# Kernel tuning notes

Measured on AMD Instinct MI355X. Metric: run time of the kernel, lower is better.

The kernel has to match this reference:

```python
import jax, jax.numpy as jnp
import numpy as np

SEQ_LENGTH = 4096
HIDDEN = 4096
N_HEADS = 32
N_KV = 2
HEAD_DIM = 128
ROT_DIM = 64  # head_dim // 2, rotary applied to first half
FFN = 13696
EPS = 1e-5


def rope_cache(seq_len):
    theta = 1.0 / (10000.0 ** (jnp.arange(0, ROT_DIM, 2, dtype=jnp.float32) / ROT_DIM))  # [32]
    idx = jnp.arange(seq_len, dtype=jnp.float32)
    freqs = jnp.outer(idx, theta)  # [seq, 32]
    return jnp.stack([jnp.cos(freqs), jnp.sin(freqs)], axis=-1)  # [seq, 32, 2]


def apply_rope(x, rope):
    # x: [sq, b, nh, 128]; rope: [sq, b, 32, 2]
    sq, b, nh, hn = x.shape
    xr = x[..., :ROT_DIM].reshape(sq, b, nh, ROT_DIM // 2, 2)
    x0, x1 = xr[..., 0], xr[..., 1]
    cos = rope[:, :, None, :, 0]
    sin = rope[:, :, None, :, 1]
    out = jnp.stack([x0 * cos - x1 * sin, x1 * cos + x0 * sin], axis=-1)
    out = out.reshape(sq, b, nh, ROT_DIM)
    return jnp.concatenate([out, x[..., ROT_DIM:]], axis=-1)


def rmsnorm(x, w):
    var = jnp.mean(jnp.square(x), axis=-1, keepdims=True)
    return x * jax.lax.rsqrt(var + EPS) * w


def setup_inputs() -> dict:
    key = jax.random.key(0)
    ks = jax.random.split(key, 12)
    B, L = 32, SEQ_LENGTH - 1
    s = 0.02
    return {
        'hidden_states': jax.random.normal(ks[0], (1, B, HIDDEN), jnp.float32),
        'position_ids': jax.random.randint(ks[1], (B, 1), 0, SEQ_LENGTH),
        'attention_mask': jnp.zeros((B, 1, 1, SEQ_LENGTH), dtype=bool),
        'past_k': jax.random.normal(ks[2], (L, B, N_KV, HEAD_DIM), jnp.float32),
        'past_v': jax.random.normal(ks[3], (L, B, N_KV, HEAD_DIM), jnp.float32),
        'w_ln1': 1.0 + s * jax.random.normal(ks[4], (HIDDEN,), jnp.float32),
        'w_qkv': s * jax.random.normal(ks[5], (HIDDEN + 2 * N_KV * HEAD_DIM, HIDDEN), jnp.float32),
        'b_qkv': s * jax.random.normal(ks[6], (HIDDEN + 2 * N_KV * HEAD_DIM,), jnp.float32),
        'w_dense': s * jax.random.normal(ks[7], (HIDDEN, HIDDEN), jnp.float32),
        'w_ln2': 1.0 + s * jax.random.normal(ks[8], (HIDDEN,), jnp.float32),
        'w_fc1': s * jax.random.normal(ks[9], (2 * FFN, HIDDEN), jnp.float32),
        'w_fc2': s * jax.random.normal(ks[10], (HIDDEN, FFN), jnp.float32),
    }


def reference(hidden_states, position_ids, attention_mask, past_k, past_v,
              w_ln1, w_qkv, b_qkv, w_dense, w_ln2, w_fc1, w_fc2):
    sq, B, _ = hidden_states.shape
    # rotary_pos_emb(SEQ_LENGTH)[position_ids].transpose(0, 1)
    rope = rope_cache(SEQ_LENGTH)[position_ids]          # [B, sq, 32, 2]
    rope = jnp.transpose(rope, (1, 0, 2, 3))             # [sq, B, 32, 2]

    # --- self attention ---
    residual = hidden_states
    x = rmsnorm(hidden_states, w_ln1)
    qkv = jnp.einsum('sbh,oh->sbo', x, w_qkv) + b_qkv    # [sq, B, 4608]
    q = qkv[..., :HIDDEN].reshape(sq, B, N_HEADS, HEAD_DIM)
    k = qkv[..., HIDDEN:HIDDEN + N_KV * HEAD_DIM].reshape(sq, B, N_KV, HEAD_DIM)
    v = qkv[..., HIDDEN + N_KV * HEAD_DIM:].reshape(sq, B, N_KV, HEAD_DIM)
    q = apply_rope(q, rope)
    k = apply_rope(k, rope)

    k_cache = jnp.concatenate([past_k, k], axis=0)       # [L+sq, B, 2, 128]
    v_cache = jnp.concatenate([past_v, v], axis=0)

    rep = N_HEADS // N_KV
    kx = jnp.repeat(k_cache, rep, axis=2)                # [sk, B, 32, 128]
    vx = jnp.repeat(v_cache, rep, axis=2)

    scale = 1.0 / jnp.sqrt(jnp.float32(HEAD_DIM))
    scores = jnp.einsum('qbhd,kbhd->bhqk', q, kx) * scale  # [B, 32, sq, sk]
    scores = jnp.where(attention_mask, jnp.float32(-1e9), scores)
    probs = jax.nn.softmax(scores, axis=-1)
    ctx = jnp.einsum('bhqk,kbhd->qbhd', probs, vx).reshape(sq, B, HIDDEN)
    attn_out = jnp.einsum('sbh,oh->sbo', ctx, w_dense)

    hidden = residual + attn_out

    # --- MLP (SwiGLU) ---
    residual = hidden
    x = rmsnorm(hidden, w_ln2)
    h = jnp.einsum('sbh,oh->sbo', x, w_fc1)              # [sq, B, 2*FFN]
    a, b = jnp.split(h, 2, axis=-1)
    h = jax.nn.silu(a) * b
    mlp_out = jnp.einsum('sbf,of->sbo', h, w_fc2)
    hidden = residual + mlp_out

    return hidden, k_cache[1:], v_cache[1:]
```

## Files before the change

kernel.cpp:

```cpp
#include <hip/hip_runtime.h>


constexpr int B    = 32;
constexpr int HID  = 4096;
constexpr int NKV  = 2;
constexpr int HD   = 128;
constexpr int QKVN = 4608;
constexpr int FFN  = 13696;
constexpr int FC1N = 2 * FFN;
constexpr int PAST = 4095;
constexpr int NSPL = 8;

constexpr size_t OFF_X1    = 0;
constexpr size_t OFF_QKVP  = OFF_X1    + (size_t)B * HID;
constexpr size_t OFF_Q     = OFF_QKVP  + 4ull * B * QKVN;
constexpr size_t OFF_KN    = OFF_Q     + (size_t)B * HID;
constexpr size_t OFF_VN    = OFF_KN    + (size_t)B * NKV * HD;
constexpr size_t OFF_CTXP  = OFF_VN    + (size_t)B * NKV * HD;
constexpr size_t OFF_ML    = OFF_CTXP  + (size_t)B * NKV * NSPL * 16 * HD;
constexpr size_t OFF_CTX   = OFF_ML    + (size_t)B * NKV * NSPL * 16 * 2;
constexpr size_t OFF_DENSP = OFF_CTX   + (size_t)B * HID;
constexpr size_t OFF_HID   = OFF_DENSP + 4ull * B * HID;
constexpr size_t OFF_X2    = OFF_HID   + (size_t)B * HID;
constexpr size_t OFF_H1    = OFF_X2    + (size_t)B * HID;
constexpr size_t OFF_HG    = OFF_H1    + 2ull * B * FC1N;
constexpr size_t OFF_FC2P  = OFF_HG    + (size_t)B * FFN;

__global__ __launch_bounds__(256) void k_rmsnorm(
    const float* __restrict__ x, const float* __restrict__ w,
    float* __restrict__ out)
{
  const int b = blockIdx.x, t = threadIdx.x;
  const float* xr = x + (size_t)b * HID;
  float4 v[4];
  float ss = 0.f;
#pragma unroll
  for (int r = 0; r < 4; r++) {
    v[r] = *(const float4*)&xr[(t + r * 256) * 4];
    ss += v[r].x * v[r].x + v[r].y * v[r].y + v[r].z * v[r].z + v[r].w * v[r].w;
  }
#pragma unroll
  for (int off = 32; off; off >>= 1) ss += __shfl_xor(ss, off);
  __shared__ float wsum[4];
  if ((t & 63) == 0) wsum[t >> 6] = ss;
  __syncthreads();
  const float tot = wsum[0] + wsum[1] + wsum[2] + wsum[3];
  const float inv = rsqrtf(tot * (1.f / HID) + 1e-5f);
  float* orow = out + (size_t)b * HID;
#pragma unroll
  for (int r = 0; r < 4; r++) {
    const int i = (t + r * 256) * 4;
    const float4 wv = *(const float4*)&w[i];
    float4 o;
    o.x = v[r].x * inv * wv.x;
    o.y = v[r].y * inv * wv.y;
    o.z = v[r].z * inv * wv.z;
    o.w = v[r].w * inv * wv.w;
    *(float4*)&orow[i] = o;
  }
}

__global__ __launch_bounds__(256) void k_resid_norm(
    const float* __restrict__ hs, const float* __restrict__ dpart,
    const float* __restrict__ w, float* __restrict__ hid,
    float* __restrict__ out)
{
  const int b = blockIdx.x, t = threadIdx.x;
  float4 v[4];
  float ss = 0.f;
#pragma unroll
  for (int r = 0; r < 4; r++) {
    const int i = (t + r * 256) * 4;
    float4 a = *(const float4*)&hs[(size_t)b * HID + i];
#pragma unroll
    for (int s = 0; s < 4; s++) {
      const float4 p = *(const float4*)&dpart[((size_t)s * B + b) * HID + i];
      a.x += p.x; a.y += p.y; a.z += p.z; a.w += p.w;
    }
    v[r] = a;
    *(float4*)&hid[(size_t)b * HID + i] = a;
    ss += a.x * a.x + a.y * a.y + a.z * a.z + a.w * a.w;
  }
#pragma unroll
  for (int off = 32; off; off >>= 1) ss += __shfl_xor(ss, off);
  __shared__ float wsum[4];
  if ((t & 63) == 0) wsum[t >> 6] = ss;
  __syncthreads();
  const float tot = wsum[0] + wsum[1] + wsum[2] + wsum[3];
  const float inv = rsqrtf(tot * (1.f / HID) + 1e-5f);
#pragma unroll
  for (int r = 0; r < 4; r++) {
    const int i = (t + r * 256) * 4;
    const float4 wv = *(const float4*)&w[i];
    float4 o;
    o.x = v[r].x * inv * wv.x;
    o.y = v[r].y * inv * wv.y;
    o.z = v[r].z * inv * wv.z;
    o.w = v[r].w * inv * wv.w;
    *(float4*)&out[(size_t)b * HID + i] = o;
  }
}

__global__ __launch_bounds__(256, 2) void k_gemv32(
    const float* __restrict__ A, const float* __restrict__ W,
    const float* __restrict__ bias, float* __restrict__ outp,
    int N, int K, int ksplit_len)
{
  __shared__ __align__(16) float xs[8192];
  const int t = threadIdx.x;
  const int wv = t >> 6, l = t & 63;
  const int olane = l >> 2, kq = l & 3;
  const int bh = wv & 1, kh = wv >> 1;
  const int o_base = blockIdx.x * 64;
  const int kb = blockIdx.y * ksplit_len;
  const int ke = kb + ksplit_len;

  float acc[4][16];
#pragma unroll
  for (int j = 0; j < 4; j++)
#pragma unroll
    for (int bb = 0; bb < 16; bb++) acc[j][bb] = 0.f;

  const float* Wr[4];
#pragma unroll
  for (int j = 0; j < 4; j++)
    Wr[j] = W + (size_t)(o_base + olane + 16 * j) * K;

  for (int kc = kb; kc < ke; kc += 256) {
    const int csz = min(256, ke - kc);
    const int c4n = csz >> 2;
    __syncthreads();
#pragma unroll
    for (int r = 0; r < 8; r++) {
      const int f = t + r * 256;
      const int b = f >> 6, c4 = f & 63;
      if (c4 < c4n)
        *(float4*)&xs[b * 256 + c4 * 4] =
            *(const float4*)&A[(size_t)b * K + kc + c4 * 4];
    }
    __syncthreads();
#pragma unroll
    for (int i = 0; i < 8; i++) {
      const int kl = kh * 128 + i * 16 + kq * 4;
      if (kl < csz) {
        float4 w4[4];
#pragma unroll
        for (int j = 0; j < 4; j++) w4[j] = *(const float4*)&Wr[j][kc + kl];
#pragma unroll
        for (int bb = 0; bb < 16; bb++) {
          const float4 xv = *(const float4*)&xs[(bh * 16 + bb) * 256 + kl];
#pragma unroll
          for (int j = 0; j < 4; j++)
            acc[j][bb] += w4[j].x * xv.x + w4[j].y * xv.y +
                          w4[j].z * xv.z + w4[j].w * xv.w;
        }
      }
    }
  }
#pragma unroll
  for (int j = 0; j < 4; j++)
#pragma unroll
    for (int bb = 0; bb < 16; bb++) {
      float v = acc[j][bb];
      v += __shfl_xor(v, 1);
      v += __shfl_xor(v, 2);
      acc[j][bb] = v;
    }
  __syncthreads();
  if (kq == 0) {
#pragma unroll
    for (int j = 0; j < 4; j++)
#pragma unroll
      for (int bb = 0; bb < 16; bb++)
        xs[(wv * 64 + olane + 16 * j) * 16 + bb] = acc[j][bb];
  }
  __syncthreads();
#pragma unroll
  for (int r = 0; r < 8; r++) {
    const int pair = t + r * 256;
    const int rl = pair >> 5, b = pair & 31;
    const int bh2 = b >> 4, bb2 = b & 15;
    float v = xs[(bh2 * 64 + rl) * 16 + bb2] +
              xs[((bh2 + 2) * 64 + rl) * 16 + bb2];
    if (bias != nullptr && blockIdx.y == 0) v += bias[o_base + rl];
    outp[((size_t)blockIdx.y * B + b) * N + o_base + rl] = v;
  }
}

__global__ __launch_bounds__(256) void k_qkv_rope(
    const float* __restrict__ qkvp, const int* __restrict__ pos_ids,
    float* __restrict__ qo, float* __restrict__ ko, float* __restrict__ vo)
{
  const int idx = blockIdx.x * 256 + threadIdx.x;
  const int b = idx / 1152;
  const int f4 = idx - b * 1152;
  const int o = f4 * 4;
  float4 v = {0.f, 0.f, 0.f, 0.f};
#pragma unroll
  for (int s = 0; s < 4; s++) {
    const float4 p = *(const float4*)&qkvp[((size_t)s * B + b) * QKVN + o];
    v.x += p.x; v.y += p.y; v.z += p.z; v.w += p.w;
  }
  const int d = o & 127;
  if (o < HID + NKV * HD && d < 64) {
    const int pos = pos_ids[b];
    const int i0 = d >> 1;
    const float f0 = pos * __expf(-0.28782313662425572f * i0);
    const float f1 = pos * __expf(-0.28782313662425572f * (i0 + 1));
    float c0, s0, c1, s1;
    sincosf(f0, &s0, &c0);
    sincosf(f1, &s1, &c1);
    float4 r;
    r.x = v.x * c0 - v.y * s0;
    r.y = v.y * c0 + v.x * s0;
    r.z = v.z * c1 - v.w * s1;
    r.w = v.w * c1 + v.z * s1;
    v = r;
  }
  if (o < HID) {
    *(float4*)&qo[(size_t)b * HID + o] = v;
  } else if (o < HID + NKV * HD) {
    *(float4*)&ko[(size_t)b * (NKV * HD) + (o - HID)] = v;
  } else {
    *(float4*)&vo[(size_t)b * (NKV * HD) + (o - HID - NKV * HD)] = v;
  }
}

__global__ __launch_bounds__(256) void k_cache_copy(
    const float4* __restrict__ pk, const float4* __restrict__ pv,
    const float4* __restrict__ kn, const float4* __restrict__ vn,
    float4* __restrict__ ok, float4* __restrict__ ov)
{
  constexpr int ROW4 = B * NKV * HD / 4;
  constexpr long long MAIN = (long long)(PAST - 1) * ROW4;
  constexpr long long TAIL = ROW4;
  const long long total = 2 * (MAIN + TAIL);
  for (long long i = (long long)blockIdx.x * 256 + threadIdx.x; i < total;
       i += (long long)gridDim.x * 256) {
    if (i < MAIN) {
      ok[i] = pk[i + ROW4];
    } else if (i < MAIN + TAIL) {
      ok[i] = kn[i - MAIN];
    } else if (i < 2 * MAIN + TAIL) {
      const long long j = i - (MAIN + TAIL);
      ov[j] = pv[j + ROW4];
    } else {
      const long long j = i - (MAIN + TAIL);
      ov[j] = vn[i - (2 * MAIN + TAIL)];
    }
  }
}

__global__ __launch_bounds__(256) void k_attn_partial(
    const float* __restrict__ q, const float* __restrict__ past_k,
    const float* __restrict__ past_v, const float* __restrict__ kn,
    const float* __restrict__ vn, float* __restrict__ ctxp,
    float* __restrict__ mlbuf)
{
  __shared__ __align__(16) float qs[16 * 128];
  __shared__ __align__(16) float sc[512 * 20];
  const int t = threadIdx.x;
  const int split = blockIdx.x, kvh = blockIdx.y, b = blockIdx.z;

#pragma unroll
  for (int r = 0; r < 2; r++) {
    const int f4 = t + r * 256;
    const int hh = f4 >> 5, d4 = f4 & 31;
    *(float4*)&qs[hh * 128 + d4 * 4] =
        *(const float4*)&q[(size_t)b * HID + (kvh * 16 + hh) * HD + d4 * 4];
  }
  __syncthreads();

  const float scale = 0.08838834764831845f;
#pragma unroll
  for (int pi = 0; pi < 2; pi++) {
    const int pl = t + pi * 256;
    const int pg = split * 512 + pl;
    const float* kr = (pg < PAST)
        ? &past_k[(size_t)((pg * B + b) * NKV + kvh) * HD]
        : &kn[(size_t)(b * NKV + kvh) * HD];
    float s[16];
#pragma unroll
    for (int hh = 0; hh < 16; hh++) s[hh] = 0.f;
#pragma unroll 4
    for (int d4 = 0; d4 < 32; d4++) {
      const float4 kv = *(const float4*)&kr[d4 * 4];
#pragma unroll
      for (int hh = 0; hh < 16; hh++) {
        const float4 q4 = *(const float4*)&qs[hh * 128 + d4 * 4];
        s[hh] += q4.x * kv.x + q4.y * kv.y + q4.z * kv.z + q4.w * kv.w;
      }
    }
#pragma unroll
    for (int hh = 0; hh < 16; hh++) sc[pl * 20 + hh] = s[hh] * scale;
  }
  __syncthreads();

  {
    const int hh = t >> 4, l16 = t & 15;
    float m = -1e30f;
    for (int jj = 0; jj < 32; jj++)
      m = fmaxf(m, sc[(l16 + jj * 16) * 20 + hh]);
#pragma unroll
    for (int off = 8; off; off >>= 1) m = fmaxf(m, __shfl_xor(m, off));
    float lsum = 0.f;
    for (int jj = 0; jj < 32; jj++) {
      const int p = l16 + jj * 16;
      const float e = __expf(sc[p * 20 + hh] - m);
      sc[p * 20 + hh] = e;
      lsum += e;
    }
#pragma unroll
    for (int off = 8; off; off >>= 1) lsum += __shfl_xor(lsum, off);
    if (l16 == 0) {
      const size_t base =
          (((size_t)(b * NKV + kvh) * NSPL + split) * 16 + hh) * 2;
      mlbuf[base] = m;
      mlbuf[base + 1] = lsum;
    }
  }
  __syncthreads();

  const int hg = t >> 7, d = t & 127;
  float acc[8];
#pragma unroll
  for (int k8 = 0; k8 < 8; k8++) acc[k8] = 0.f;
  for (int pl = 0; pl < 512; pl++) {
    const int pg = split * 512 + pl;
    const float vd = (pg < PAST)
        ? past_v[(size_t)((pg * B + b) * NKV + kvh) * HD + d]
        : vn[(size_t)(b * NKV + kvh) * HD + d];
    const float4 e0 = *(const float4*)&sc[pl * 20 + hg * 8];
    const float4 e1 = *(const float4*)&sc[pl * 20 + hg * 8 + 4];
    acc[0] += e0.x * vd; acc[1] += e0.y * vd;
    acc[2] += e0.z * vd; acc[3] += e0.w * vd;
    acc[4] += e1.x * vd; acc[5] += e1.y * vd;
    acc[6] += e1.z * vd; acc[7] += e1.w * vd;
  }
#pragma unroll
  for (int k8 = 0; k8 < 8; k8++) {
    const size_t idx =
        (((size_t)(b * NKV + kvh) * NSPL + split) * 16 + hg * 8 + k8) * HD + d;
    ctxp[idx] = acc[k8];
  }
}

__global__ __launch_bounds__(128) void k_attn_merge(
    const float* __restrict__ ctxp, const float* __restrict__ mlbuf,
    float* __restrict__ ctx)
{
  const int h = blockIdx.x, b = blockIdx.y, d = threadIdx.x;
  const int kvh = h >> 4, hh = h & 15;
  float ms[NSPL], ls[NSPL];
  float M = -1e30f;
#pragma unroll
  for (int s = 0; s < NSPL; s++) {
    const size_t base = (((size_t)(b * NKV + kvh) * NSPL + s) * 16 + hh) * 2;
    ms[s] = mlbuf[base];
    ls[s] = mlbuf[base + 1];
    M = fmaxf(M, ms[s]);
  }
  float L = 0.f, val = 0.f;
#pragma unroll
  for (int s = 0; s < NSPL; s++) {
    const float w = __expf(ms[s] - M);
    L += ls[s] * w;
    val += w * ctxp[(((size_t)(b * NKV + kvh) * NSPL + s) * 16 + hh) * HD + d];
  }
  ctx[(size_t)b * HID + h * HD + d] = val / L;
}

__global__ __launch_bounds__(256) void k_swiglu(
    const float* __restrict__ h1p, float* __restrict__ hg)
{
  const int idx = blockIdx.x * 256 + threadIdx.x;
  const int b = idx / 3424;
  const int f4 = idx - b * 3424;
  float4 a = *(const float4*)&h1p[(size_t)b * FC1N + f4 * 4];
  float4 g = *(const float4*)&h1p[(size_t)b * FC1N + FFN + f4 * 4];
  const float4 a1 = *(const float4*)&h1p[((size_t)B + b) * FC1N + f4 * 4];
  const float4 g1 = *(const float4*)&h1p[((size_t)B + b) * FC1N + FFN + f4 * 4];
  a.x += a1.x; a.y += a1.y; a.z += a1.z; a.w += a1.w;
  g.x += g1.x; g.y += g1.y; g.z += g1.z; g.w += g1.w;
  float4 o;
  o.x = a.x / (1.f + __expf(-a.x)) * g.x;
  o.y = a.y / (1.f + __expf(-a.y)) * g.y;
  o.z = a.z / (1.f + __expf(-a.z)) * g.z;
  o.w = a.w / (1.f + __expf(-a.w)) * g.w;
  *(float4*)&hg[(size_t)b * FFN + f4 * 4] = o;
}

__global__ __launch_bounds__(256) void k_final(
    const float* __restrict__ hid, const float* __restrict__ fp,
    float* __restrict__ out)
{
  const int idx = blockIdx.x * 256 + threadIdx.x;
  const int b = idx >> 10, i4 = idx & 1023;
  float4 v = *(const float4*)&hid[(size_t)b * HID + i4 * 4];
#pragma unroll
  for (int s = 0; s < 4; s++) {
    const float4 p = *(const float4*)&fp[((size_t)s * B + b) * HID + i4 * 4];
    v.x += p.x; v.y += p.y; v.z += p.z; v.w += p.w;
  }
  *(float4*)&out[(size_t)b * HID + i4 * 4] = v;
}

extern "C" void kernel_launch(void* const* d_in, const int* in_sizes, int n_in,
                              void* d_out, int out_size, void* d_ws,
                              size_t ws_size, hipStream_t stream)
{
  const float* hs     = (const float*)d_in[0];
  const int*   pos    = (const int*)  d_in[1];
  const float* pk     = (const float*)d_in[3];
  const float* pv     = (const float*)d_in[4];
  const float* wln1   = (const float*)d_in[5];
  const float* wqkv   = (const float*)d_in[6];
  const float* bqkv   = (const float*)d_in[7];
  const float* wdense = (const float*)d_in[8];
  const float* wln2   = (const float*)d_in[9];
  const float* wfc1   = (const float*)d_in[10];
  const float* wfc2   = (const float*)d_in[11];

  float* ws  = (float*)d_ws;
  float* out = (float*)d_out;

  float* x1    = ws + OFF_X1;
  float* qkvp  = ws + OFF_QKVP;
  float* q     = ws + OFF_Q;
  float* kn    = ws + OFF_KN;
  float* vn    = ws + OFF_VN;
  float* ctxp  = ws + OFF_CTXP;
  float* mlbuf = ws + OFF_ML;
  float* ctx   = ws + OFF_CTX;
  float* densp = ws + OFF_DENSP;
  float* hid   = ws + OFF_HID;
  float* x2    = ws + OFF_X2;
  float* h1    = ws + OFF_H1;
  float* hg    = ws + OFF_HG;
  float* fc2p  = ws + OFF_FC2P;

  float* out_k = out + (size_t)B * HID;
  float* out_v = out_k + (size_t)PAST * B * NKV * HD;

  hipLaunchKernelGGL(k_rmsnorm, dim3(B), dim3(256), 0, stream, hs, wln1, x1);
  hipLaunchKernelGGL(k_gemv32, dim3(QKVN / 64, 4), dim3(256), 0, stream,
                     x1, wqkv, bqkv, qkvp, QKVN, HID, HID / 4);
  hipLaunchKernelGGL(k_qkv_rope, dim3(144), dim3(256), 0, stream,
                     qkvp, pos, q, kn, vn);
  hipLaunchKernelGGL(k_cache_copy, dim3(4096), dim3(256), 0, stream,
                     (const float4*)pk, (const float4*)pv,
                     (const float4*)kn, (const float4*)vn,
                     (float4*)out_k, (float4*)out_v);
  hipLaunchKernelGGL(k_attn_partial, dim3(NSPL, NKV, B), dim3(256), 0, stream,
                     q, pk, pv, kn, vn, ctxp, mlbuf);
  hipLaunchKernelGGL(k_attn_merge, dim3(32, 32), dim3(128), 0, stream,
                     ctxp, mlbuf, ctx);
  hipLaunchKernelGGL(k_gemv32, dim3(HID / 64, 4), dim3(256), 0, stream,
                     ctx, wdense, (const float*)nullptr, densp, HID, HID,
                     HID / 4);
  hipLaunchKernelGGL(k_resid_norm, dim3(B), dim3(256), 0, stream,
                     hs, densp, wln2, hid, x2);
  hipLaunchKernelGGL(k_gemv32, dim3(FC1N / 64, 2), dim3(256), 0, stream,
                     x2, wfc1, (const float*)nullptr, h1, FC1N, HID, HID / 2);
  hipLaunchKernelGGL(k_swiglu, dim3(428), dim3(256), 0, stream, h1, hg);
  hipLaunchKernelGGL(k_gemv32, dim3(HID / 64, 4), dim3(256), 0, stream,
                     hg, wfc2, (const float*)nullptr, fc2p, HID, FFN, FFN / 4);
  hipLaunchKernelGGL(k_final, dim3(128), dim3(256), 0, stream, hid, fc2p, out);
}
```

Measured before the change: 628.0 us.

## Fuse KV cache copy into attention and raise split-K for GEMVs

Drops the separate cache-copy kernel. The attention kernel now writes the shifted K/V cache rows to the output as it reads them for the dot products, so the past cache is read from HBM once instead of twice. The QKV, dense and FC2 GEMVs now use 8 split-K slices instead of 4 to put more blocks in flight, and one shared workspace buffer holds all the partial sums, with the reducers summing 8 partials. The costs are scattered writes inside the attention loop and extra traffic for reducing the partials.

```diff
diff --git a/kernel.cpp b/kernel.cpp
--- a/kernel.cpp
+++ b/kernel.cpp
@@ -11,20 +11,18 @@
 constexpr int PAST = 4095;
 constexpr int NSPL = 8;
 
-constexpr size_t OFF_X1    = 0;
-constexpr size_t OFF_QKVP  = OFF_X1    + (size_t)B * HID;
-constexpr size_t OFF_Q     = OFF_QKVP  + 4ull * B * QKVN;
-constexpr size_t OFF_KN    = OFF_Q     + (size_t)B * HID;
-constexpr size_t OFF_VN    = OFF_KN    + (size_t)B * NKV * HD;
-constexpr size_t OFF_CTXP  = OFF_VN    + (size_t)B * NKV * HD;
-constexpr size_t OFF_ML    = OFF_CTXP  + (size_t)B * NKV * NSPL * 16 * HD;
-constexpr size_t OFF_CTX   = OFF_ML    + (size_t)B * NKV * NSPL * 16 * 2;
-constexpr size_t OFF_DENSP = OFF_CTX   + (size_t)B * HID;
-constexpr size_t OFF_HID   = OFF_DENSP + 4ull * B * HID;
-constexpr size_t OFF_X2    = OFF_HID   + (size_t)B * HID;
-constexpr size_t OFF_H1    = OFF_X2    + (size_t)B * HID;
-constexpr size_t OFF_HG    = OFF_H1    + 2ull * B * FC1N;
-constexpr size_t OFF_FC2P  = OFF_HG    + (size_t)B * FFN;
+constexpr size_t OFF_X1   = 0;
+constexpr size_t OFF_P    = OFF_X1   + (size_t)B * HID;
+constexpr size_t P_SIZE   = 2ull * B * FC1N;
+constexpr size_t OFF_Q    = OFF_P    + P_SIZE;
+constexpr size_t OFF_KN   = OFF_Q    + (size_t)B * HID;
+constexpr size_t OFF_VN   = OFF_KN   + (size_t)B * NKV * HD;
+constexpr size_t OFF_CTXP = OFF_VN   + (size_t)B * NKV * HD;
+constexpr size_t OFF_ML   = OFF_CTXP + (size_t)B * NKV * NSPL * 16 * HD;
+constexpr size_t OFF_CTX  = OFF_ML   + (size_t)B * NKV * NSPL * 16 * 2;
+constexpr size_t OFF_HID  = OFF_CTX  + (size_t)B * HID;
+constexpr size_t OFF_X2   = OFF_HID  + (size_t)B * HID;
+constexpr size_t OFF_HG   = OFF_X2   + (size_t)B * HID;
 
 __global__ __launch_bounds__(256) void k_rmsnorm(
     const float* __restrict__ x, const float* __restrict__ w,
@@ -73,7 +71,7 @@
     const int i = (t + r * 256) * 4;
     float4 a = *(const float4*)&hs[(size_t)b * HID + i];
 #pragma unroll
-    for (int s = 0; s < 4; s++) {
+    for (int s = 0; s < 8; s++) {
       const float4 p = *(const float4*)&dpart[((size_t)s * B + b) * HID + i];
       a.x += p.x; a.y += p.y; a.z += p.z; a.w += p.w;
     }
@@ -197,7 +195,7 @@
   const int o = f4 * 4;
   float4 v = {0.f, 0.f, 0.f, 0.f};
 #pragma unroll
-  for (int s = 0; s < 4; s++) {
+  for (int s = 0; s < 8; s++) {
     const float4 p = *(const float4*)&qkvp[((size_t)s * B + b) * QKVN + o];
     v.x += p.x; v.y += p.y; v.z += p.z; v.w += p.w;
   }
@@ -226,35 +224,11 @@
   }
 }
 
-__global__ __launch_bounds__(256) void k_cache_copy(
-    const float4* __restrict__ pk, const float4* __restrict__ pv,
-    const float4* __restrict__ kn, const float4* __restrict__ vn,
-    float4* __restrict__ ok, float4* __restrict__ ov)
-{
-  constexpr int ROW4 = B * NKV * HD / 4;
-  constexpr long long MAIN = (long long)(PAST - 1) * ROW4;
-  constexpr long long TAIL = ROW4;
-  const long long total = 2 * (MAIN + TAIL);
-  for (long long i = (long long)blockIdx.x * 256 + threadIdx.x; i < total;
-       i += (long long)gridDim.x * 256) {
-    if (i < MAIN) {
-      ok[i] = pk[i + ROW4];
-    } else if (i < MAIN + TAIL) {
-      ok[i] = kn[i - MAIN];
-    } else if (i < 2 * MAIN + TAIL) {
-      const long long j = i - (MAIN + TAIL);
-      ov[j] = pv[j + ROW4];
-    } else {
-      const long long j = i - (MAIN + TAIL);
-      ov[j] = vn[i - (2 * MAIN + TAIL)];
-    }
-  }
-}
-
 __global__ __launch_bounds__(256) void k_attn_partial(
     const float* __restrict__ q, const float* __restrict__ past_k,
     const float* __restrict__ past_v, const float* __restrict__ kn,
-    const float* __restrict__ vn, float* __restrict__ ctxp,
+    const float* __restrict__ vn, float* __restrict__ ok,
+    float* __restrict__ ov, float* __restrict__ ctxp,
     float* __restrict__ mlbuf)
 {
   __shared__ __align__(16) float qs[16 * 128];
@@ -279,12 +253,16 @@
     const float* kr = (pg < PAST)
         ? &past_k[(size_t)((pg * B + b) * NKV + kvh) * HD]
         : &kn[(size_t)(b * NKV + kvh) * HD];
+    float4* kw = (pg >= 1)
+        ? (float4*)&ok[(((size_t)(pg - 1) * B + b) * NKV + kvh) * HD]
+        : nullptr;
     float s[16];
 #pragma unroll
     for (int hh = 0; hh < 16; hh++) s[hh] = 0.f;
 #pragma unroll 4
     for (int d4 = 0; d4 < 32; d4++) {
       const float4 kv = *(const float4*)&kr[d4 * 4];
+      if (kw) kw[d4] = kv;
 #pragma unroll
       for (int hh = 0; hh < 16; hh++) {
         const float4 q4 = *(const float4*)&qs[hh * 128 + d4 * 4];
@@ -330,6 +308,8 @@
     const float vd = (pg < PAST)
         ? past_v[(size_t)((pg * B + b) * NKV + kvh) * HD + d]
         : vn[(size_t)(b * NKV + kvh) * HD + d];
+    if (hg == 0 && pg >= 1)
+      ov[(((size_t)(pg - 1) * B + b) * NKV + kvh) * HD + d] = vd;
     const float4 e0 = *(const float4*)&sc[pl * 20 + hg * 8];
     const float4 e1 = *(const float4*)&sc[pl * 20 + hg * 8 + 4];
     acc[0] += e0.x * vd; acc[1] += e0.y * vd;
@@ -398,7 +378,7 @@
   const int b = idx >> 10, i4 = idx & 1023;
   float4 v = *(const float4*)&hid[(size_t)b * HID + i4 * 4];
 #pragma unroll
-  for (int s = 0; s < 4; s++) {
+  for (int s = 0; s < 8; s++) {
     const float4 p = *(const float4*)&fp[((size_t)s * B + b) * HID + i4 * 4];
     v.x += p.x; v.y += p.y; v.z += p.z; v.w += p.w;
   }
@@ -425,45 +405,37 @@
   float* out = (float*)d_out;
 
   float* x1    = ws + OFF_X1;
-  float* qkvp  = ws + OFF_QKVP;
+  float* P     = ws + OFF_P;
   float* q     = ws + OFF_Q;
   float* kn    = ws + OFF_KN;
   float* vn    = ws + OFF_VN;
   float* ctxp  = ws + OFF_CTXP;
   float* mlbuf = ws + OFF_ML;
   float* ctx   = ws + OFF_CTX;
-  float* densp = ws + OFF_DENSP;
   float* hid   = ws + OFF_HID;
   float* x2    = ws + OFF_X2;
-  float* h1    = ws + OFF_H1;
   float* hg    = ws + OFF_HG;
-  float* fc2p  = ws + OFF_FC2P;
 
   float* out_k = out + (size_t)B * HID;
   float* out_v = out_k + (size_t)PAST * B * NKV * HD;
 
   hipLaunchKernelGGL(k_rmsnorm, dim3(B), dim3(256), 0, stream, hs, wln1, x1);
-  hipLaunchKernelGGL(k_gemv32, dim3(QKVN / 64, 4), dim3(256), 0, stream,
-                     x1, wqkv, bqkv, qkvp, QKVN, HID, HID / 4);
+  hipLaunchKernelGGL(k_gemv32, dim3(QKVN / 64, 8), dim3(256), 0, stream,
+                     x1, wqkv, bqkv, P, QKVN, HID, HID / 8);
   hipLaunchKernelGGL(k_qkv_rope, dim3(144), dim3(256), 0, stream,
-                     qkvp, pos, q, kn, vn);
-  hipLaunchKernelGGL(k_cache_copy, dim3(4096), dim3(256), 0, stream,
-                     (const float4*)pk, (const float4*)pv,
-                     (const float4*)kn, (const float4*)vn,
-                     (float4*)out_k, (float4*)out_v);
+                     P, pos, q, kn, vn);
   hipLaunchKernelGGL(k_attn_partial, dim3(NSPL, NKV, B), dim3(256), 0, stream,
-                     q, pk, pv, kn, vn, ctxp, mlbuf);
+                     q, pk, pv, kn, vn, out_k, out_v, ctxp, mlbuf);
   hipLaunchKernelGGL(k_attn_merge, dim3(32, 32), dim3(128), 0, stream,
                      ctxp, mlbuf, ctx);
-  hipLaunchKernelGGL(k_gemv32, dim3(HID / 64, 4), dim3(256), 0, stream,
-                     ctx, wdense, (const float*)nullptr, densp, HID, HID,
-                     HID / 4);
+  hipLaunchKernelGGL(k_gemv32, dim3(HID / 64, 8), dim3(256), 0, stream,
+                     ctx, wdense, (const float*)nullptr, P, HID, HID, HID / 8);
   hipLaunchKernelGGL(k_resid_norm, dim3(B), dim3(256), 0, stream,
-                     hs, densp, wln2, hid, x2);
+                     hs, P, wln2, hid, x2);
   hipLaunchKernelGGL(k_gemv32, dim3(FC1N / 64, 2), dim3(256), 0, stream,
-                     x2, wfc1, (const float*)nullptr, h1, FC1N, HID, HID / 2);
-  hipLaunchKernelGGL(k_swiglu, dim3(428), dim3(256), 0, stream, h1, hg);
-  hipLaunchKernelGGL(k_gemv32, dim3(HID / 64, 4), dim3(256), 0, stream,
-                     hg, wfc2, (const float*)nullptr, fc2p, HID, FFN, FFN / 4);
-  hipLaunchKernelGGL(k_final, dim3(128), dim3(256), 0, stream, hid, fc2p, out);
-}
+                     x2, wfc1, (const float*)nullptr, P, FC1N, HID, HID / 2);
+  hipLaunchKernelGGL(k_swiglu, dim3(428), dim3(256), 0, stream, P, hg);
+  hipLaunchKernelGGL(k_gemv32, dim3(HID / 64, 8), dim3(256), 0, stream,
+                     hg, wfc2, (const float*)nullptr, P, HID, FFN, FFN / 8);
+  hipLaunchKernelGGL(k_final, dim3(128), dim3(256), 0, stream, hid, P, out);
+}
```

After: 748.2 us. 19.1% more time.
